# Kernel optimization log

Measured on AMD Instinct MI355X. Metric: run time of the kernel, lower is better.

The kernel has to match this reference:

```python
import jax, jax.numpy as jnp
import numpy as np

# Propagation forward (reference path), with:
#   pairwise_fn       = dot product over feature dim: scores[b,i,j] = <val[b,i], val[b,j]>
#   edge_compress_fn  = softsign(x) = x / (1 + |x|)
#   val_proj/state_proj = Identity, return_delta = True
# Output: concat(delta_val [B,N,D], delta_state [B,N,1]) -> [B,N,D+1]

B, N, D = 4, 4096, 256


def setup_inputs() -> dict:
    key = jax.random.key(0)
    k1, k2 = jax.random.split(key)
    val = jax.random.normal(k1, (B, N, D), dtype=jnp.float32)
    state = jax.random.normal(k2, (B, N), dtype=jnp.float32)
    return {"val": val, "state": state}


def reference(val, state):
    # pairwise scores over all node pairs: [B, N, N]
    scores = jnp.einsum("bid,bjd->bij", val, val)
    # softsign edge compression
    edges = scores / (1.0 + jnp.abs(scores))
    # delta_state[b,i] = sum_j edges[b,i,j] * state[b,j]
    delta_state = jnp.einsum("bij,bj->bi", edges, state)
    # delta_val[b,i,d] = sum_j edges[b,i,j] * val[b,j,d]
    delta_val = jnp.einsum("bij,bjd->bid", edges, val)
    return jnp.concatenate([delta_val, delta_state[..., None]], axis=-1)
```

## Files before the change

kernel.cpp:

```cpp
#include <hip/hip_runtime.h>
#include <stdint.h>

#define BATCH 4
#define NN 4096
#define DD 256
#define TI 128
#define TJ 64
#define JS 2
#define JRANGE (NN / JS)
#define NITER (JRANGE / TJ)

#define VS_OFF 0
#define VT_OFF 65536
#define P_OFF  131072
#define LDS_BYTES 163840

typedef __attribute__((ext_vector_type(8))) short bf16x8;
typedef __attribute__((ext_vector_type(4))) float f32x4;
typedef __attribute__((ext_vector_type(4))) float f4v;
typedef __attribute__((ext_vector_type(8))) short s8v;
typedef __attribute__((ext_vector_type(4))) short s4v;

__device__ __forceinline__ short f2bf(float f) {
    uint32_t u = __builtin_bit_cast(uint32_t, f);
    u = (u + 0x7fffu + ((u >> 16) & 1u)) >> 16;
    return (short)u;
}

__device__ __forceinline__ void g2l16(const void* g, void* l) {
    __builtin_amdgcn_global_load_lds((const __attribute__((address_space(1))) void*)g,
                                     (__attribute__((address_space(3))) void*)l, 16, 0, 0);
}

__global__ __launch_bounds__(256) void prep_k(const float* __restrict__ val,
                                              short* __restrict__ vbf,
                                              short* __restrict__ vt) {
    __shared__ float tile[32][33];
    int b = blockIdx.z;
    int d0 = blockIdx.x * 32, n0 = blockIdx.y * 32;
    int tx = threadIdx.x, ty = threadIdx.y;
#pragma unroll
    for (int yy = ty; yy < 32; yy += 8) {
        float v = val[((size_t)b * NN + n0 + yy) * DD + d0 + tx];
        tile[yy][tx] = v;
        vbf[((size_t)b * NN + n0 + yy) * DD + d0 + tx] = f2bf(v);
    }
    __syncthreads();
#pragma unroll
    for (int yy = ty; yy < 32; yy += 8)
        vt[((size_t)b * DD + d0 + yy) * NN + n0 + tx] = f2bf(tile[tx][yy]);
}

__global__ void __launch_bounds__(512, 2) prop_main(const short* __restrict__ vbf,
                                                    const short* __restrict__ vtbf,
                                                    const float* __restrict__ state,
                                                    float* __restrict__ part,
                                                    float* __restrict__ spart) {
    extern __shared__ char smem[];

    const int bid = blockIdx.x;
    const int js = bid & 1;
    const int rb = (bid >> 1) & 31;
    const int b = bid >> 6;
    const int tid = threadIdx.x;
    const int w = tid >> 6, lane = tid & 63;
    const int g = lane >> 4, c = lane & 15;
    const int ig = w & 3, jh = w >> 2;
    const int wr = w & 1, wd = w >> 1;
    const int r7 = c & 7;
    const int j0base = js * JRANGE;

    const int xE = ((((r7 >> 2) << 2) | (g ^ (r7 & 3))) << 4);
    const int xO = (((((r7 >> 2) ^ 1) << 2) | (g ^ (r7 & 3))) << 4);

    bf16x8 Bf[2][8];
    const size_t irowb = (size_t)b * NN + rb * TI + ig * 32;
#pragma unroll
    for (int m = 0; m < 2; ++m)
#pragma unroll
        for (int k = 0; k < 8; ++k)
            Bf[m][k] = *(const bf16x8*)(vbf + ((irowb + m * 16 + c) * DD + k * 32 + g * 8));

    f32x4 accO[4][4];
#pragma unroll
    for (int mt = 0; mt < 4; ++mt)
#pragma unroll
        for (int dt = 0; dt < 4; ++dt)
            accO[mt][dt] = (f32x4){0.f, 0.f, 0.f, 0.f};
    float vsum[2] = {0.f, 0.f};

    auto stageVs = [&](int t, int nb) {
        const int j0 = j0base + t * TJ;
        char* dst = smem + VS_OFF + nb * 32768;
#pragma unroll
        for (int p = 0; p < 4; ++p) {
            int ch0 = p * 512 + w * 64;
            int ch = ch0 + lane;
            int row = ch >> 5, cir = ch & 31;
            g2l16(vbf + ((size_t)(b * NN + j0 + row) * DD + ((cir ^ (row & 7)) * 8)),
                  dst + ch0 * 16);
        }
    };
    auto stageVt = [&](int t, int nb) {
        const int j0 = j0base + t * TJ;
        char* dst = smem + VT_OFF + nb * 32768;
#pragma unroll
        for (int p = 0; p < 4; ++p) {
            int ch0 = p * 512 + w * 64;
            int ch = ch0 + lane;
            int d = ch >> 3, cj = ch & 7;
            g2l16(vtbf + ((size_t)(b * DD + d) * NN + j0 + ((cj ^ (d & 7)) * 8)),
                  dst + ch0 * 16);
        }
    };

    auto pvStep = [&](int slot) {
        const char* paRow = smem + P_OFF + slot * 16384 + (wr * 64 + c) * 128;
        const char* vbRow = smem + VT_OFF + slot * 32768 + (wd * 64 + c) * 128;
        __builtin_amdgcn_s_setprio(1);
#pragma unroll
        for (int kk = 0; kk < 2; ++kk) {
            const int off = kk ? xO : xE;
            bf16x8 pa[4], vb[4];
#pragma unroll
            for (int mt = 0; mt < 4; ++mt) pa[mt] = *(const bf16x8*)(paRow + mt * 2048 + off);
#pragma unroll
            for (int dt = 0; dt < 4; ++dt) vb[dt] = *(const bf16x8*)(vbRow + dt * 2048 + off);
#pragma unroll
            for (int mt = 0; mt < 4; ++mt)
#pragma unroll
                for (int dt = 0; dt < 4; ++dt)
                    accO[mt][dt] = __builtin_amdgcn_mfma_f32_16x16x32_bf16(pa[mt], vb[dt], accO[mt][dt], 0, 0, 0);
        }
        __builtin_amdgcn_s_setprio(0);
    };

    const float* stp = state + b * NN + j0base;

    stageVs(0, 0);
    stageVt(0, 0);
    __syncthreads();

    for (int t = 0; t < NITER; ++t) {
        const int cur = t & 1, prv = cur ^ 1;

        if (t + 1 < NITER) stageVs(t + 1, prv);

        f4v sv0 = *(const f4v*)(stp + t * TJ + jh * 32 + g * 4);
        f4v sv1 = *(const f4v*)(stp + t * TJ + jh * 32 + 16 + g * 4);

        f32x4 accS[2][2];
#pragma unroll
        for (int jbl = 0; jbl < 2; ++jbl)
#pragma unroll
            for (int m = 0; m < 2; ++m)
                accS[jbl][m] = (f32x4){0.f, 0.f, 0.f, 0.f};

        const char* aRow0 = smem + VS_OFF + cur * 32768 + (jh * 32 + c) * 512;
#pragma unroll
        for (int k = 0; k < 8; ++k) {
            const int off = (k >> 1) * 128 + ((k & 1) ? xO : xE);
            bf16x8 a0 = *(const bf16x8*)(aRow0 + off);
            bf16x8 a1 = *(const bf16x8*)(aRow0 + 8192 + off);
            accS[0][0] = __builtin_amdgcn_mfma_f32_16x16x32_bf16(a0, Bf[0][k], accS[0][0], 0, 0, 0);
            accS[0][1] = __builtin_amdgcn_mfma_f32_16x16x32_bf16(a0, Bf[1][k], accS[0][1], 0, 0, 0);
            accS[1][0] = __builtin_amdgcn_mfma_f32_16x16x32_bf16(a1, Bf[0][k], accS[1][0], 0, 0, 0);
            accS[1][1] = __builtin_amdgcn_mfma_f32_16x16x32_bf16(a1, Bf[1][k], accS[1][1], 0, 0, 0);
        }

        if (t > 0) pvStep(prv);

#pragma unroll
        for (int jbl = 0; jbl < 2; ++jbl) {
            f4v sv = jbl ? sv1 : sv0;
#pragma unroll
            for (int m = 0; m < 2; ++m) {
                s4v pk;
#pragma unroll
                for (int r = 0; r < 4; ++r) {
                    float s = accS[jbl][m][r];
                    float e = s * __builtin_amdgcn_rcpf(1.0f + __builtin_fabsf(s));
                    vsum[m] += e * sv[r];
                    pk[r] = f2bf(e);
                }
                int i = ig * 32 + m * 16 + c;
                *(s4v*)(smem + P_OFF + cur * 16384 + i * 128 +
                        ((jh * 64 + jbl * 32 + g * 8) ^ (r7 << 4))) = pk;
            }
        }

        __syncthreads();

        if (t + 1 < NITER) stageVt(t + 1, prv);
    }

    pvStep((NITER - 1) & 1);

    {
        float* po = part + (((size_t)(js * BATCH + b) * NN + rb * TI + wr * 64) * DD) + wd * 64;
#pragma unroll
        for (int mt = 0; mt < 4; ++mt)
#pragma unroll
            for (int dt = 0; dt < 4; ++dt)
#pragma unroll
                for (int r = 0; r < 4; ++r)
                    po[(size_t)(mt * 16 + g * 4 + r) * DD + dt * 16 + c] = accO[mt][dt][r];
    }

#pragma unroll
    for (int m = 0; m < 2; ++m) {
        vsum[m] += __shfl_xor(vsum[m], 16);
        vsum[m] += __shfl_xor(vsum[m], 32);
    }
    float* Xf = (float*)(smem + P_OFF);
    __syncthreads();
    if (jh == 1 && lane < 16) {
        Xf[(ig * 2 + 0) * 16 + lane] = vsum[0];
        Xf[(ig * 2 + 1) * 16 + lane] = vsum[1];
    }
    __syncthreads();
    if (jh == 0 && lane < 16) {
        size_t sb = ((size_t)js * BATCH + b) * NN + rb * TI + ig * 32;
#pragma unroll
        for (int m = 0; m < 2; ++m)
            spart[sb + m * 16 + lane] = vsum[m] + Xf[(ig * 2 + m) * 16 + lane];
    }
}

__global__ __launch_bounds__(256) void reduce2_k(const float* __restrict__ part,
                                                 const float* __restrict__ spart,
                                                 float* __restrict__ out) {
    const int row = blockIdx.x;
    const int t = threadIdx.x;
    const size_t PS = (size_t)BATCH * NN * DD;
    float v = part[(size_t)row * DD + t] + part[PS + (size_t)row * DD + t];
    out[(size_t)row * 257 + t] = v;
    if (t == 0) {
        const size_t SS = (size_t)BATCH * NN;
        out[(size_t)row * 257 + 256] = spart[row] + spart[SS + row];
    }
}

extern "C" void kernel_launch(void* const* d_in, const int* in_sizes, int n_in,
                              void* d_out, int out_size, void* d_ws, size_t ws_size,
                              hipStream_t stream) {
    const float* val = (const float*)d_in[0];
    const float* state = (const float*)d_in[1];
    float* out = (float*)d_out;

    const size_t bf_bytes = (size_t)BATCH * NN * DD * 2;
    const size_t part_bytes = (size_t)JS * BATCH * NN * DD * 4;
    const size_t spart_bytes = (size_t)JS * BATCH * NN * 4;
    short* vbf = (short*)d_ws;
    short* vtbf = (short*)((char*)d_ws + bf_bytes);
    float* part = (float*)((char*)d_ws + 2 * bf_bytes);
    float* spart = (float*)((char*)d_ws + 2 * bf_bytes + part_bytes);
    if (ws_size < 2 * bf_bytes + part_bytes + spart_bytes) return;

    hipFuncSetAttribute((const void*)prop_main, hipFuncAttributeMaxDynamicSharedMemorySize, LDS_BYTES);

    prep_k<<<dim3(DD / 32, NN / 32, BATCH), dim3(32, 8), 0, stream>>>(val, vbf, vtbf);
    prop_main<<<BATCH * (NN / TI) * JS, 512, LDS_BYTES, stream>>>(vbf, vtbf, state, part, spart);
    reduce2_k<<<BATCH * NN, 256, 0, stream>>>(part, spart, out);
}
```

Baseline: 93.38 us.

## Retile score warps to 64 i-rows per warp and store bf16 partials

The score phase now gives each warp 64 i-rows (four held B fragments) and 16 j-columns instead of 32x32. Each LDS A-fragment load therefore feeds four MFMAs, which cuts LDS reads of the staged V tile, at the cost of more registers for the held fragments. The split-j partial outputs are written as bf16 instead of fp32, halving partial-sum traffic in the main kernel's store and in the reduce kernel. The PV step is reordered to load P fragments in pairs, and the state-sum reduction is rewritten for four j-quarter warps.

```diff
diff --git a/kernel.cpp b/kernel.cpp
--- a/kernel.cpp
+++ b/kernel.cpp
@@ -18,13 +18,16 @@
 typedef __attribute__((ext_vector_type(8))) short bf16x8;
 typedef __attribute__((ext_vector_type(4))) float f32x4;
 typedef __attribute__((ext_vector_type(4))) float f4v;
-typedef __attribute__((ext_vector_type(8))) short s8v;
 typedef __attribute__((ext_vector_type(4))) short s4v;
 
 __device__ __forceinline__ short f2bf(float f) {
     uint32_t u = __builtin_bit_cast(uint32_t, f);
     u = (u + 0x7fffu + ((u >> 16) & 1u)) >> 16;
     return (short)u;
+}
+__device__ __forceinline__ float bf2f(unsigned short u) {
+    uint32_t x = ((uint32_t)u) << 16;
+    return __builtin_bit_cast(float, x);
 }
 
 __device__ __forceinline__ void g2l16(const void* g, void* l) {
@@ -54,7 +57,7 @@
 __global__ void __launch_bounds__(512, 2) prop_main(const short* __restrict__ vbf,
                                                     const short* __restrict__ vtbf,
                                                     const float* __restrict__ state,
-                                                    float* __restrict__ part,
+                                                    unsigned short* __restrict__ part,
                                                     float* __restrict__ spart) {
     extern __shared__ char smem[];
 
@@ -65,7 +68,7 @@
     const int tid = threadIdx.x;
     const int w = tid >> 6, lane = tid & 63;
     const int g = lane >> 4, c = lane & 15;
-    const int ig = w & 3, jh = w >> 2;
+    const int jq = w & 3, ih = w >> 2;
     const int wr = w & 1, wd = w >> 1;
     const int r7 = c & 7;
     const int j0base = js * JRANGE;
@@ -73,10 +76,10 @@
     const int xE = ((((r7 >> 2) << 2) | (g ^ (r7 & 3))) << 4);
     const int xO = (((((r7 >> 2) ^ 1) << 2) | (g ^ (r7 & 3))) << 4);
 
-    bf16x8 Bf[2][8];
-    const size_t irowb = (size_t)b * NN + rb * TI + ig * 32;
-#pragma unroll
-    for (int m = 0; m < 2; ++m)
+    bf16x8 Bf[4][8];
+    const size_t irowb = (size_t)b * NN + rb * TI + ih * 64;
+#pragma unroll
+    for (int m = 0; m < 4; ++m)
 #pragma unroll
         for (int k = 0; k < 8; ++k)
             Bf[m][k] = *(const bf16x8*)(vbf + ((irowb + m * 16 + c) * DD + k * 32 + g * 8));
@@ -87,7 +90,7 @@
 #pragma unroll
         for (int dt = 0; dt < 4; ++dt)
             accO[mt][dt] = (f32x4){0.f, 0.f, 0.f, 0.f};
-    float vsum[2] = {0.f, 0.f};
+    float vsum[4] = {0.f, 0.f, 0.f, 0.f};
 
     auto stageVs = [&](int t, int nb) {
         const int j0 = j0base + t * TJ;
@@ -121,16 +124,19 @@
 #pragma unroll
         for (int kk = 0; kk < 2; ++kk) {
             const int off = kk ? xO : xE;
-            bf16x8 pa[4], vb[4];
-#pragma unroll
-            for (int mt = 0; mt < 4; ++mt) pa[mt] = *(const bf16x8*)(paRow + mt * 2048 + off);
+            bf16x8 vb[4];
 #pragma unroll
             for (int dt = 0; dt < 4; ++dt) vb[dt] = *(const bf16x8*)(vbRow + dt * 2048 + off);
 #pragma unroll
-            for (int mt = 0; mt < 4; ++mt)
-#pragma unroll
-                for (int dt = 0; dt < 4; ++dt)
-                    accO[mt][dt] = __builtin_amdgcn_mfma_f32_16x16x32_bf16(pa[mt], vb[dt], accO[mt][dt], 0, 0, 0);
+            for (int mp = 0; mp < 2; ++mp) {
+                bf16x8 pa0 = *(const bf16x8*)(paRow + (mp * 2 + 0) * 2048 + off);
+                bf16x8 pa1 = *(const bf16x8*)(paRow + (mp * 2 + 1) * 2048 + off);
+#pragma unroll
+                for (int dt = 0; dt < 4; ++dt) {
+                    accO[mp * 2 + 0][dt] = __builtin_amdgcn_mfma_f32_16x16x32_bf16(pa0, vb[dt], accO[mp * 2 + 0][dt], 0, 0, 0);
+                    accO[mp * 2 + 1][dt] = __builtin_amdgcn_mfma_f32_16x16x32_bf16(pa1, vb[dt], accO[mp * 2 + 1][dt], 0, 0, 0);
+                }
+            }
         }
         __builtin_amdgcn_s_setprio(0);
     };
@@ -146,47 +152,38 @@
 
         if (t + 1 < NITER) stageVs(t + 1, prv);
 
-        f4v sv0 = *(const f4v*)(stp + t * TJ + jh * 32 + g * 4);
-        f4v sv1 = *(const f4v*)(stp + t * TJ + jh * 32 + 16 + g * 4);
-
-        f32x4 accS[2][2];
-#pragma unroll
-        for (int jbl = 0; jbl < 2; ++jbl)
-#pragma unroll
-            for (int m = 0; m < 2; ++m)
-                accS[jbl][m] = (f32x4){0.f, 0.f, 0.f, 0.f};
-
-        const char* aRow0 = smem + VS_OFF + cur * 32768 + (jh * 32 + c) * 512;
+        f4v sv = *(const f4v*)(stp + t * TJ + jq * 16 + g * 4);
+
+        f32x4 accS[4];
+#pragma unroll
+        for (int m = 0; m < 4; ++m) accS[m] = (f32x4){0.f, 0.f, 0.f, 0.f};
+
+        const char* aRow0 = smem + VS_OFF + cur * 32768 + (jq * 16 + c) * 512;
 #pragma unroll
         for (int k = 0; k < 8; ++k) {
             const int off = (k >> 1) * 128 + ((k & 1) ? xO : xE);
             bf16x8 a0 = *(const bf16x8*)(aRow0 + off);
-            bf16x8 a1 = *(const bf16x8*)(aRow0 + 8192 + off);
-            accS[0][0] = __builtin_amdgcn_mfma_f32_16x16x32_bf16(a0, Bf[0][k], accS[0][0], 0, 0, 0);
-            accS[0][1] = __builtin_amdgcn_mfma_f32_16x16x32_bf16(a0, Bf[1][k], accS[0][1], 0, 0, 0);
-            accS[1][0] = __builtin_amdgcn_mfma_f32_16x16x32_bf16(a1, Bf[0][k], accS[1][0], 0, 0, 0);
-            accS[1][1] = __builtin_amdgcn_mfma_f32_16x16x32_bf16(a1, Bf[1][k], accS[1][1], 0, 0, 0);
+            accS[0] = __builtin_amdgcn_mfma_f32_16x16x32_bf16(a0, Bf[0][k], accS[0], 0, 0, 0);
+            accS[1] = __builtin_amdgcn_mfma_f32_16x16x32_bf16(a0, Bf[1][k], accS[1], 0, 0, 0);
+            accS[2] = __builtin_amdgcn_mfma_f32_16x16x32_bf16(a0, Bf[2][k], accS[2], 0, 0, 0);
+            accS[3] = __builtin_amdgcn_mfma_f32_16x16x32_bf16(a0, Bf[3][k], accS[3], 0, 0, 0);
         }
 
         if (t > 0) pvStep(prv);
 
 #pragma unroll
-        for (int jbl = 0; jbl < 2; ++jbl) {
-            f4v sv = jbl ? sv1 : sv0;
-#pragma unroll
-            for (int m = 0; m < 2; ++m) {
-                s4v pk;
-#pragma unroll
-                for (int r = 0; r < 4; ++r) {
-                    float s = accS[jbl][m][r];
-                    float e = s * __builtin_amdgcn_rcpf(1.0f + __builtin_fabsf(s));
-                    vsum[m] += e * sv[r];
-                    pk[r] = f2bf(e);
-                }
-                int i = ig * 32 + m * 16 + c;
-                *(s4v*)(smem + P_OFF + cur * 16384 + i * 128 +
-                        ((jh * 64 + jbl * 32 + g * 8) ^ (r7 << 4))) = pk;
+        for (int m = 0; m < 4; ++m) {
+            s4v pk;
+#pragma unroll
+            for (int r = 0; r < 4; ++r) {
+                float s = accS[m][r];
+                float e = s * __builtin_amdgcn_rcpf(1.0f + __builtin_fabsf(s));
+                vsum[m] += e * sv[r];
+                pk[r] = f2bf(e);
             }
+            int i = ih * 64 + m * 16 + c;
+            *(s4v*)(smem + P_OFF + cur * 16384 + i * 128 +
+                    ((jq * 32 + g * 8) ^ (r7 << 4))) = pk;
         }
 
         __syncthreads();
@@ -197,43 +194,50 @@
     pvStep((NITER - 1) & 1);
 
     {
-        float* po = part + (((size_t)(js * BATCH + b) * NN + rb * TI + wr * 64) * DD) + wd * 64;
+        unsigned short* po = part + (((size_t)(js * BATCH + b) * NN + rb * TI + wr * 64) * DD) + wd * 64;
 #pragma unroll
         for (int mt = 0; mt < 4; ++mt)
 #pragma unroll
             for (int dt = 0; dt < 4; ++dt)
 #pragma unroll
                 for (int r = 0; r < 4; ++r)
-                    po[(size_t)(mt * 16 + g * 4 + r) * DD + dt * 16 + c] = accO[mt][dt][r];
-    }
-
-#pragma unroll
-    for (int m = 0; m < 2; ++m) {
+                    po[(size_t)(mt * 16 + g * 4 + r) * DD + dt * 16 + c] =
+                        (unsigned short)f2bf(accO[mt][dt][r]);
+    }
+
+#pragma unroll
+    for (int m = 0; m < 4; ++m) {
         vsum[m] += __shfl_xor(vsum[m], 16);
         vsum[m] += __shfl_xor(vsum[m], 32);
     }
     float* Xf = (float*)(smem + P_OFF);
     __syncthreads();
-    if (jh == 1 && lane < 16) {
-        Xf[(ig * 2 + 0) * 16 + lane] = vsum[0];
-        Xf[(ig * 2 + 1) * 16 + lane] = vsum[1];
-    }
-    __syncthreads();
-    if (jh == 0 && lane < 16) {
-        size_t sb = ((size_t)js * BATCH + b) * NN + rb * TI + ig * 32;
-#pragma unroll
-        for (int m = 0; m < 2; ++m)
-            spart[sb + m * 16 + lane] = vsum[m] + Xf[(ig * 2 + m) * 16 + lane];
-    }
-}
-
-__global__ __launch_bounds__(256) void reduce2_k(const float* __restrict__ part,
+    if (lane < 16) {
+#pragma unroll
+        for (int m = 0; m < 4; ++m)
+            Xf[((jq * 2 + ih) * 4 + m) * 16 + lane] = vsum[m];
+    }
+    __syncthreads();
+    if (jq == 0 && lane < 16) {
+        size_t sb = ((size_t)js * BATCH + b) * NN + rb * TI + ih * 64;
+#pragma unroll
+        for (int m = 0; m < 4; ++m) {
+            float acc = 0.f;
+#pragma unroll
+            for (int q = 0; q < 4; ++q)
+                acc += Xf[((q * 2 + ih) * 4 + m) * 16 + lane];
+            spart[sb + m * 16 + lane] = acc;
+        }
+    }
+}
+
+__global__ __launch_bounds__(256) void reduce2_k(const unsigned short* __restrict__ part,
                                                  const float* __restrict__ spart,
                                                  float* __restrict__ out) {
     const int row = blockIdx.x;
     const int t = threadIdx.x;
     const size_t PS = (size_t)BATCH * NN * DD;
-    float v = part[(size_t)row * DD + t] + part[PS + (size_t)row * DD + t];
+    float v = bf2f(part[(size_t)row * DD + t]) + bf2f(part[PS + (size_t)row * DD + t]);
     out[(size_t)row * 257 + t] = v;
     if (t == 0) {
         const size_t SS = (size_t)BATCH * NN;
@@ -249,11 +253,11 @@
     float* out = (float*)d_out;
 
     const size_t bf_bytes = (size_t)BATCH * NN * DD * 2;
-    const size_t part_bytes = (size_t)JS * BATCH * NN * DD * 4;
+    const size_t part_bytes = (size_t)JS * BATCH * NN * DD * 2;
     const size_t spart_bytes = (size_t)JS * BATCH * NN * 4;
     short* vbf = (short*)d_ws;
     short* vtbf = (short*)((char*)d_ws + bf_bytes);
-    float* part = (float*)((char*)d_ws + 2 * bf_bytes);
+    unsigned short* part = (unsigned short*)((char*)d_ws + 2 * bf_bytes);
     float* spart = (float*)((char*)d_ws + 2 * bf_bytes + part_bytes);
     if (ws_size < 2 * bf_bytes + part_bytes + spart_bytes) return;
 
```

After: 158.8 us. +70.0%, slower.

## Halve tile sizes to 64x32 with 256-thread blocks and remapped block order

Applied to the files above, without the earlier changes.

Shrinks the row tile from 128 to 64 and the j tile from 64 to 32, runs 4 waves per block instead of 8, and reworks the LDS layouts, swizzles and warp-to-work mapping to match. Blocks are remapped so consecutive block IDs are spread across batches and row blocks, likely for better L2 or XCD locality. The grid grows to 512 blocks with less LDS each, which raises occupancy and fills more CUs. The cost is less data reuse per block, twice the global staging traffic per FLOP, and more loop iterations with barriers.

```diff
diff --git a/kernel.cpp b/kernel.cpp
--- a/kernel.cpp
+++ b/kernel.cpp
@@ -4,21 +4,20 @@
 #define BATCH 4
 #define NN 4096
 #define DD 256
-#define TI 128
-#define TJ 64
+#define TI 64
+#define TJ 32
 #define JS 2
 #define JRANGE (NN / JS)
 #define NITER (JRANGE / TJ)
 
 #define VS_OFF 0
-#define VT_OFF 65536
-#define P_OFF  131072
-#define LDS_BYTES 163840
+#define VT_OFF 32768
+#define P_OFF  65536
+#define LDS_BYTES 73728
 
 typedef __attribute__((ext_vector_type(8))) short bf16x8;
 typedef __attribute__((ext_vector_type(4))) float f32x4;
 typedef __attribute__((ext_vector_type(4))) float f4v;
-typedef __attribute__((ext_vector_type(8))) short s8v;
 typedef __attribute__((ext_vector_type(4))) short s4v;
 
 __device__ __forceinline__ short f2bf(float f) {
@@ -51,30 +50,33 @@
         vt[((size_t)b * DD + d0 + yy) * NN + n0 + tx] = f2bf(tile[tx][yy]);
 }
 
-__global__ void __launch_bounds__(512, 2) prop_main(const short* __restrict__ vbf,
+__global__ void __launch_bounds__(256, 2) prop_main(const short* __restrict__ vbf,
                                                     const short* __restrict__ vtbf,
                                                     const float* __restrict__ state,
                                                     float* __restrict__ part,
                                                     float* __restrict__ spart) {
     extern __shared__ char smem[];
 
-    const int bid = blockIdx.x;
+    const int raw = blockIdx.x;
+    const int bid = ((raw & 7) << 6) | (raw >> 3);
     const int js = bid & 1;
-    const int rb = (bid >> 1) & 31;
-    const int b = bid >> 6;
+    const int rb = (bid >> 1) & 63;
+    const int b = bid >> 7;
     const int tid = threadIdx.x;
     const int w = tid >> 6, lane = tid & 63;
     const int g = lane >> 4, c = lane & 15;
-    const int ig = w & 3, jh = w >> 2;
-    const int wr = w & 1, wd = w >> 1;
+    const int jh = w & 1, ih = w >> 1;
+    const int dq = w;
     const int r7 = c & 7;
+    const int c3 = c & 3;
     const int j0base = js * JRANGE;
 
     const int xE = ((((r7 >> 2) << 2) | (g ^ (r7 & 3))) << 4);
     const int xO = (((((r7 >> 2) ^ 1) << 2) | (g ^ (r7 & 3))) << 4);
+    const int offQ = (g ^ c3) << 4;
 
     bf16x8 Bf[2][8];
-    const size_t irowb = (size_t)b * NN + rb * TI + ig * 32;
+    const size_t irowb = (size_t)b * NN + rb * TI + ih * 32;
 #pragma unroll
     for (int m = 0; m < 2; ++m)
 #pragma unroll
@@ -91,10 +93,10 @@
 
     auto stageVs = [&](int t, int nb) {
         const int j0 = j0base + t * TJ;
-        char* dst = smem + VS_OFF + nb * 32768;
+        char* dst = smem + VS_OFF + nb * 16384;
 #pragma unroll
         for (int p = 0; p < 4; ++p) {
-            int ch0 = p * 512 + w * 64;
+            int ch0 = p * 256 + w * 64;
             int ch = ch0 + lane;
             int row = ch >> 5, cir = ch & 31;
             g2l16(vbf + ((size_t)(b * NN + j0 + row) * DD + ((cir ^ (row & 7)) * 8)),
@@ -103,35 +105,31 @@
     };
     auto stageVt = [&](int t, int nb) {
         const int j0 = j0base + t * TJ;
-        char* dst = smem + VT_OFF + nb * 32768;
+        char* dst = smem + VT_OFF + nb * 16384;
 #pragma unroll
         for (int p = 0; p < 4; ++p) {
-            int ch0 = p * 512 + w * 64;
+            int ch0 = p * 256 + w * 64;
             int ch = ch0 + lane;
-            int d = ch >> 3, cj = ch & 7;
-            g2l16(vtbf + ((size_t)(b * DD + d) * NN + j0 + ((cj ^ (d & 7)) * 8)),
+            int d = ch >> 2, sl = ch & 3;
+            g2l16(vtbf + ((size_t)(b * DD + d) * NN + j0 + ((sl ^ (d & 3)) * 8)),
                   dst + ch0 * 16);
         }
     };
 
     auto pvStep = [&](int slot) {
-        const char* paRow = smem + P_OFF + slot * 16384 + (wr * 64 + c) * 128;
-        const char* vbRow = smem + VT_OFF + slot * 32768 + (wd * 64 + c) * 128;
+        const char* paRow = smem + P_OFF + slot * 4096 + c * 64 + offQ;
+        const char* vbRow = smem + VT_OFF + slot * 16384 + (dq * 64 + c) * 64 + offQ;
         __builtin_amdgcn_s_setprio(1);
-#pragma unroll
-        for (int kk = 0; kk < 2; ++kk) {
-            const int off = kk ? xO : xE;
-            bf16x8 pa[4], vb[4];
-#pragma unroll
-            for (int mt = 0; mt < 4; ++mt) pa[mt] = *(const bf16x8*)(paRow + mt * 2048 + off);
-#pragma unroll
-            for (int dt = 0; dt < 4; ++dt) vb[dt] = *(const bf16x8*)(vbRow + dt * 2048 + off);
-#pragma unroll
-            for (int mt = 0; mt < 4; ++mt)
-#pragma unroll
-                for (int dt = 0; dt < 4; ++dt)
-                    accO[mt][dt] = __builtin_amdgcn_mfma_f32_16x16x32_bf16(pa[mt], vb[dt], accO[mt][dt], 0, 0, 0);
-        }
+        bf16x8 pa[4], vb[4];
+#pragma unroll
+        for (int mt = 0; mt < 4; ++mt) pa[mt] = *(const bf16x8*)(paRow + mt * 1024);
+#pragma unroll
+        for (int dt = 0; dt < 4; ++dt) vb[dt] = *(const bf16x8*)(vbRow + dt * 1024);
+#pragma unroll
+        for (int mt = 0; mt < 4; ++mt)
+#pragma unroll
+            for (int dt = 0; dt < 4; ++dt)
+                accO[mt][dt] = __builtin_amdgcn_mfma_f32_16x16x32_bf16(pa[mt], vb[dt], accO[mt][dt], 0, 0, 0);
         __builtin_amdgcn_s_setprio(0);
     };
 
@@ -146,47 +144,36 @@
 
         if (t + 1 < NITER) stageVs(t + 1, prv);
 
-        f4v sv0 = *(const f4v*)(stp + t * TJ + jh * 32 + g * 4);
-        f4v sv1 = *(const f4v*)(stp + t * TJ + jh * 32 + 16 + g * 4);
-
-        f32x4 accS[2][2];
-#pragma unroll
-        for (int jbl = 0; jbl < 2; ++jbl)
-#pragma unroll
-            for (int m = 0; m < 2; ++m)
-                accS[jbl][m] = (f32x4){0.f, 0.f, 0.f, 0.f};
-
-        const char* aRow0 = smem + VS_OFF + cur * 32768 + (jh * 32 + c) * 512;
+        f4v sv = *(const f4v*)(stp + t * TJ + jh * 16 + g * 4);
+
+        f32x4 accS[2];
+        accS[0] = (f32x4){0.f, 0.f, 0.f, 0.f};
+        accS[1] = (f32x4){0.f, 0.f, 0.f, 0.f};
+
+        const char* aRow0 = smem + VS_OFF + cur * 16384 + (jh * 16 + c) * 512;
 #pragma unroll
         for (int k = 0; k < 8; ++k) {
             const int off = (k >> 1) * 128 + ((k & 1) ? xO : xE);
             bf16x8 a0 = *(const bf16x8*)(aRow0 + off);
-            bf16x8 a1 = *(const bf16x8*)(aRow0 + 8192 + off);
-            accS[0][0] = __builtin_amdgcn_mfma_f32_16x16x32_bf16(a0, Bf[0][k], accS[0][0], 0, 0, 0);
-            accS[0][1] = __builtin_amdgcn_mfma_f32_16x16x32_bf16(a0, Bf[1][k], accS[0][1], 0, 0, 0);
-            accS[1][0] = __builtin_amdgcn_mfma_f32_16x16x32_bf16(a1, Bf[0][k], accS[1][0], 0, 0, 0);
-            accS[1][1] = __builtin_amdgcn_mfma_f32_16x16x32_bf16(a1, Bf[1][k], accS[1][1], 0, 0, 0);
+            accS[0] = __builtin_amdgcn_mfma_f32_16x16x32_bf16(a0, Bf[0][k], accS[0], 0, 0, 0);
+            accS[1] = __builtin_amdgcn_mfma_f32_16x16x32_bf16(a0, Bf[1][k], accS[1], 0, 0, 0);
         }
 
         if (t > 0) pvStep(prv);
 
 #pragma unroll
-        for (int jbl = 0; jbl < 2; ++jbl) {
-            f4v sv = jbl ? sv1 : sv0;
-#pragma unroll
-            for (int m = 0; m < 2; ++m) {
-                s4v pk;
-#pragma unroll
-                for (int r = 0; r < 4; ++r) {
-                    float s = accS[jbl][m][r];
-                    float e = s * __builtin_amdgcn_rcpf(1.0f + __builtin_fabsf(s));
-                    vsum[m] += e * sv[r];
-                    pk[r] = f2bf(e);
-                }
-                int i = ig * 32 + m * 16 + c;
-                *(s4v*)(smem + P_OFF + cur * 16384 + i * 128 +
-                        ((jh * 64 + jbl * 32 + g * 8) ^ (r7 << 4))) = pk;
+        for (int m = 0; m < 2; ++m) {
+            s4v pk;
+#pragma unroll
+            for (int r = 0; r < 4; ++r) {
+                float s = accS[m][r];
+                float e = s * __builtin_amdgcn_rcpf(1.0f + __builtin_fabsf(s));
+                vsum[m] += e * sv[r];
+                pk[r] = f2bf(e);
             }
+            int i = ih * 32 + m * 16 + c;
+            *(s4v*)(smem + P_OFF + cur * 4096 + i * 64 +
+                    ((((jh << 1) | (g >> 1)) ^ c3) << 4) + ((g & 1) << 3)) = pk;
         }
 
         __syncthreads();
@@ -197,7 +184,7 @@
     pvStep((NITER - 1) & 1);
 
     {
-        float* po = part + (((size_t)(js * BATCH + b) * NN + rb * TI + wr * 64) * DD) + wd * 64;
+        float* po = part + (((size_t)(js * BATCH + b) * NN + rb * TI) * DD) + dq * 64;
 #pragma unroll
         for (int mt = 0; mt < 4; ++mt)
 #pragma unroll
@@ -215,15 +202,15 @@
     float* Xf = (float*)(smem + P_OFF);
     __syncthreads();
     if (jh == 1 && lane < 16) {
-        Xf[(ig * 2 + 0) * 16 + lane] = vsum[0];
-        Xf[(ig * 2 + 1) * 16 + lane] = vsum[1];
+        Xf[(ih * 2 + 0) * 16 + lane] = vsum[0];
+        Xf[(ih * 2 + 1) * 16 + lane] = vsum[1];
     }
     __syncthreads();
     if (jh == 0 && lane < 16) {
-        size_t sb = ((size_t)js * BATCH + b) * NN + rb * TI + ig * 32;
+        size_t sb = ((size_t)js * BATCH + b) * NN + rb * TI + ih * 32;
 #pragma unroll
         for (int m = 0; m < 2; ++m)
-            spart[sb + m * 16 + lane] = vsum[m] + Xf[(ig * 2 + m) * 16 + lane];
+            spart[sb + m * 16 + lane] = vsum[m] + Xf[(ih * 2 + m) * 16 + lane];
     }
 }
 
@@ -260,6 +247,6 @@
     hipFuncSetAttribute((const void*)prop_main, hipFuncAttributeMaxDynamicSharedMemorySize, LDS_BYTES);
 
     prep_k<<<dim3(DD / 32, NN / 32, BATCH), dim3(32, 8), 0, stream>>>(val, vbf, vtbf);
-    prop_main<<<BATCH * (NN / TI) * JS, 512, LDS_BYTES, stream>>>(vbf, vtbf, state, part, spart);
+    prop_main<<<BATCH * (NN / TI) * JS, 256, LDS_BYTES, stream>>>(vbf, vtbf, state, part, spart);
     reduce2_k<<<BATCH * NN, 256, 0, stream>>>(part, spart, out);
 }
```

Measured after the change: 107.2 us. +14.8%, slower.
